# Kernel optimization log

Hardware: AMD Instinct MI355X
Metric: run time of the kernel (lower is better)

The kernel has to match this reference:

```python
import jax, jax.numpy as jnp
import numpy as np

NEG_SLOPE = 0.2  # DenseGATConv default negative_slope


def dense_gat(x, adj, W, att_src, att_dst, bias):
    # x: [B,N,Cin], adj: [B,N,N] (self-loops already added), W: [Cin,H*C]
    B, N, _ = x.shape
    H, C = att_src.shape
    h = (x @ W).reshape(B, N, H, C)
    a_src = jnp.einsum('bnhc,hc->bnh', h, att_src)  # [B,N,H]
    a_dst = jnp.einsum('bnhc,hc->bnh', h, att_dst)
    # alpha[b,i,j,h] = a_src[b,j,h] + a_dst[b,i,h]  (softmax over j, axis=2)
    alpha = a_src[:, None, :, :] + a_dst[:, :, None, :]
    alpha = jnp.where(alpha >= 0, alpha, NEG_SLOPE * alpha)  # leaky_relu
    mask = (adj != 0)[..., None]  # [B,N,N,1]
    alpha = jax.nn.softmax(jnp.where(mask, alpha, -1e30), axis=2)
    out = jnp.einsum('bijh,bjhc->bihc', alpha, h).reshape(B, N, H * C)
    return out + bias


def setup_inputs() -> dict:
    key = jax.random.key(0)
    ks = jax.random.split(key, 8)
    B, N, D = 1, 8192, 128
    x = jax.random.normal(ks[0], (B, N, D), dtype=jnp.float32)
    adj = (jax.random.uniform(ks[1], (B, N, N)) < 0.01).astype(jnp.float32)
    idx = jnp.arange(N)
    adj = adj.at[:, idx, idx].set(1.0)  # DenseGATConv add_loop=True
    s = 1.0 / np.sqrt(D)
    lin = lambda k: jax.random.uniform(k, (D, D), minval=-s, maxval=s, dtype=jnp.float32)
    att = lambda k: jax.random.normal(k, (1, D), dtype=jnp.float32) * 0.1  # heads=1
    return dict(
        x=x, adj=adj,
        W0=lin(ks[2]), att_src0=att(ks[3]), att_dst0=att(ks[4]), b0=jnp.zeros((D,), jnp.float32),
        W1=lin(ks[5]), att_src1=att(ks[6]), att_dst1=att(ks[7]), b1=jnp.zeros((D,), jnp.float32),
    )


def reference(x, adj, W0, att_src0, att_dst0, b0, W1, att_src1, att_dst1, b1):
    out0 = dense_gat(x, adj, W0, att_src0, att_dst0, b0)
    out0 = jax.nn.relu(out0)  # relu_layers_index = [0]
    out1 = dense_gat(out0, adj, W1, att_src1, att_dst1, b1)
    # dropout_rate = 0 -> dropout is identity; squeeze batch dim as in block
    return (out0[0], out1[0])
```

## Files before the change

### kernel.cpp

```cpp
#include <hip/hip_runtime.h>

#define MAXDEG 192
#define NEG_SLOPE 0.2f
#define D 128

__device__ __forceinline__ float bf2f(unsigned short u) {
    return __uint_as_float(((unsigned)u) << 16);
}
__device__ __forceinline__ unsigned short f2bf(float f) {
    unsigned u = __float_as_uint(f);
    return (unsigned short)((u + 0x7fffu + ((u >> 16) & 1u)) >> 16);
}
__device__ __forceinline__ unsigned pack2bf(float x, float y) {
    return (unsigned)f2bf(x) | ((unsigned)f2bf(y) << 16);
}
__device__ __forceinline__ int is_f32(const void* adj) {
    return ((const unsigned*)adj)[0] == 0x3F800000u;
}

__device__ __forceinline__ void ell_group(
        int g, const void* __restrict__ adj, int N, int f32m,
        unsigned short* __restrict__ cols, int* __restrict__ deg,
        int* __restrict__ cnt ) {
    const int w = threadIdx.x >> 6, lane = threadIdx.x & 63;
    const int row = g * 4 + w;
    if (lane == 0) cnt[w] = 0;
    __syncthreads();
    unsigned short* crow = cols + (size_t)row * MAXDEG;
    if (f32m) {
        const float4* arow = (const float4*)((const float*)adj + (size_t)row * N);
        const int nv = N / 4;
        for (int v = lane; v < nv; v += 128) {
            float4 u0 = arow[v];
            float4 u1 = arow[v + 64];
            const unsigned* a0 = (const unsigned*)&u0;
            const unsigned* a1 = (const unsigned*)&u1;
            #pragma unroll
            for (int e = 0; e < 4; e++)
                if (a0[e]) { int p = atomicAdd(&cnt[w], 1); if (p < MAXDEG) crow[p] = (unsigned short)(v * 4 + e); }
            #pragma unroll
            for (int e = 0; e < 4; e++)
                if (a1[e]) { int p = atomicAdd(&cnt[w], 1); if (p < MAXDEG) crow[p] = (unsigned short)((v + 64) * 4 + e); }
        }
    } else {
        const uint4* arow = (const uint4*)((const unsigned short*)adj + (size_t)row * N);
        const int nv = N / 8;
        for (int v = lane; v < nv; v += 128) {
            uint4 u0 = arow[v];
            uint4 u1 = arow[v + 64];
            const unsigned short* s0 = (const unsigned short*)&u0;
            const unsigned short* s1 = (const unsigned short*)&u1;
            #pragma unroll
            for (int e = 0; e < 8; e++)
                if (s0[e]) { int p = atomicAdd(&cnt[w], 1); if (p < MAXDEG) crow[p] = (unsigned short)(v * 8 + e); }
            #pragma unroll
            for (int e = 0; e < 8; e++)
                if (s1[e]) { int p = atomicAdd(&cnt[w], 1); if (p < MAXDEG) crow[p] = (unsigned short)((v + 64) * 8 + e); }
        }
    }
    __syncthreads();
    if (lane == 0) deg[row] = cnt[w] < MAXDEG ? cnt[w] : MAXDEG;
}

__device__ __forceinline__ void gemm_tile32(
        int t, const void* __restrict__ A, const void* __restrict__ W,
        int aF, int f32m, const void* __restrict__ attS, const void* __restrict__ attD,
        unsigned short* __restrict__ Hb, float* __restrict__ asrc, float* __restrict__ adst,
        float* __restrict__ smem) {
    float* xs = smem;
    float* ws = smem + 4096;
    const int tid = threadIdx.x;
    const size_t row0 = (size_t)t * 32;

    if (aF) {
        const float4* av = (const float4*)((const float*)A + row0 * D);
        float4* xl = (float4*)xs;
        #pragma unroll
        for (int k = 0; k < 4; k++) xl[tid + 256 * k] = av[tid + 256 * k];
    } else {
        const uint4* av = (const uint4*)((const unsigned short*)A + row0 * D);
        #pragma unroll
        for (int k = 0; k < 2; k++) {
            uint4 u = av[tid + 256 * k];
            const unsigned short* us = (const unsigned short*)&u;
            #pragma unroll
            for (int e = 0; e < 8; e++) xs[(tid + 256 * k) * 8 + e] = bf2f(us[e]);
        }
    }

    const int tx = tid & 31, ty = tid >> 5;
    const int c0 = tx * 4, r0 = ty * 4;
    float acc[4][4] = {};
    for (int p = 0; p < 4; p++) {
        __syncthreads();
        if (f32m) {
            const float4* wv = (const float4*)((const float*)W + (size_t)p * 32 * D);
            float4* wl = (float4*)ws;
            #pragma unroll
            for (int k = 0; k < 4; k++) wl[tid + 256 * k] = wv[tid + 256 * k];
        } else {
            const uint4* wv = (const uint4*)((const unsigned short*)W + (size_t)p * 32 * D);
            #pragma unroll
            for (int k = 0; k < 2; k++) {
                uint4 u = wv[tid + 256 * k];
                const unsigned short* us = (const unsigned short*)&u;
                #pragma unroll
                for (int e = 0; e < 8; e++) ws[(tid + 256 * k) * 8 + e] = bf2f(us[e]);
            }
        }
        __syncthreads();
        #pragma unroll 8
        for (int k = 0; k < 32; k++) {
            float4 wv = *(const float4*)&ws[k * D + c0];
            #pragma unroll
            for (int i = 0; i < 4; i++) {
                float xv = xs[(r0 + i) * D + p * 32 + k];
                acc[i][0] += xv * wv.x; acc[i][1] += xv * wv.y;
                acc[i][2] += xv * wv.z; acc[i][3] += xv * wv.w;
            }
        }
    }
    #pragma unroll
    for (int i = 0; i < 4; i++) {
        ushort4 hv;
        hv.x = f2bf(acc[i][0]); hv.y = f2bf(acc[i][1]);
        hv.z = f2bf(acc[i][2]); hv.w = f2bf(acc[i][3]);
        *(ushort4*)&Hb[(row0 + r0 + i) * D + c0] = hv;
    }

    float aSv[4], aDv[4];
    #pragma unroll
    for (int j = 0; j < 4; j++) {
        aSv[j] = f32m ? ((const float*)attS)[c0 + j] : bf2f(((const unsigned short*)attS)[c0 + j]);
        aDv[j] = f32m ? ((const float*)attD)[c0 + j] : bf2f(((const unsigned short*)attD)[c0 + j]);
    }
    #pragma unroll
    for (int i = 0; i < 4; i++) {
        float s = acc[i][0] * aSv[0] + acc[i][1] * aSv[1] + acc[i][2] * aSv[2] + acc[i][3] * aSv[3];
        float d = acc[i][0] * aDv[0] + acc[i][1] * aDv[1] + acc[i][2] * aDv[2] + acc[i][3] * aDv[3];
        #pragma unroll
        for (int off = 16; off > 0; off >>= 1) {
            s += __shfl_down(s, off, 32);
            d += __shfl_down(d, off, 32);
        }
        if (tx == 0) {
            asrc[row0 + r0 + i] = s;
            adst[row0 + r0 + i] = d;
        }
    }
}

__device__ __forceinline__ float2 agg_row_bf(
        int row, const unsigned short* __restrict__ Hb,
        const float* __restrict__ asrc, float ai,
        const unsigned short* __restrict__ crow, int d,
        const void* __restrict__ bias, int f32m, int relu,
        float* __restrict__ scn, unsigned short* __restrict__ sjj, int lane) {
    const int s0 = lane, s1 = lane + 64, s2 = lane + 128;
    unsigned short j0 = 0, j1 = 0, j2 = 0;
    float e0 = -3e38f, e1 = -3e38f, e2 = -3e38f;
    if (s0 < d) { j0 = crow[s0]; float e = asrc[j0] + ai; e0 = (e >= 0.f) ? e : NEG_SLOPE * e; }
    if (s1 < d) { j1 = crow[s1]; float e = asrc[j1] + ai; e1 = (e >= 0.f) ? e : NEG_SLOPE * e; }
    if (s2 < d) { j2 = crow[s2]; float e = asrc[j2] + ai; e2 = (e >= 0.f) ? e : NEG_SLOPE * e; }
    float m = fmaxf(e0, fmaxf(e1, e2));
    #pragma unroll
    for (int off = 1; off < 64; off <<= 1) m = fmaxf(m, __shfl_xor(m, off));
    float p0 = (s0 < d) ? __expf(e0 - m) : 0.f;
    float p1 = (s1 < d) ? __expf(e1 - m) : 0.f;
    float p2 = (s2 < d) ? __expf(e2 - m) : 0.f;
    float l = p0 + p1 + p2;
    #pragma unroll
    for (int off = 1; off < 64; off <<= 1) l += __shfl_xor(l, off);
    const float invl = 1.f / l;
    scn[s0] = p0 * invl; sjj[s0] = j0;
    scn[s1] = p1 * invl; sjj[s1] = j1;
    scn[s2] = p2 * invl; sjj[s2] = j2;

    const unsigned* H2 = (const unsigned*)Hb;
    float ax[8], ay[8];
    #pragma unroll
    for (int u = 0; u < 8; u++) { ax[u] = 0.f; ay[u] = 0.f; }
    int k = 0;
    for (; k + 7 < d; k += 8) {
        int jj[8]; float ww[8]; unsigned vv[8];
        #pragma unroll
        for (int u = 0; u < 8; u++) { jj[u] = sjj[k + u]; ww[u] = scn[k + u]; }
        #pragma unroll
        for (int u = 0; u < 8; u++) vv[u] = H2[(size_t)jj[u] * 64 + lane];
        #pragma unroll
        for (int u = 0; u < 8; u++) {
            ax[u] += ww[u] * bf2f((unsigned short)(vv[u] & 0xffff));
            ay[u] += ww[u] * bf2f((unsigned short)(vv[u] >> 16));
        }
    }
    for (; k < d; k++) {
        const int j = sjj[k];
        const float wk = scn[k];
        unsigned v = H2[(size_t)j * 64 + lane];
        ax[0] += wk * bf2f((unsigned short)(v & 0xffff));
        ay[0] += wk * bf2f((unsigned short)(v >> 16));
    }
    #pragma unroll
    for (int u = 1; u < 8; u++) { ax[0] += ax[u]; ay[0] += ay[u]; }

    const int c0 = lane * 2;
    const float bx = f32m ? ((const float*)bias)[c0]     : bf2f(((const unsigned short*)bias)[c0]);
    const float by = f32m ? ((const float*)bias)[c0 + 1] : bf2f(((const unsigned short*)bias)[c0 + 1]);
    float vx = ax[0] + bx, vy = ay[0] + by;
    if (relu) { vx = fmaxf(vx, 0.f); vy = fmaxf(vy, 0.f); }
    return make_float2(vx, vy);
}

__global__ __launch_bounds__(256) void ell_gemm0(
        const void* __restrict__ x, const void* __restrict__ adj,
        const void* __restrict__ W0, const void* __restrict__ aS0,
        const void* __restrict__ aD0, int N,
        unsigned short* __restrict__ cols, int* __restrict__ deg,
        unsigned short* __restrict__ h, float* __restrict__ asrc, float* __restrict__ adst) {
    __shared__ float smem[8192];
    const int bid = blockIdx.x;
    const int f32m = is_f32(adj);
    const int GT = N / 32;
    if (bid < GT)
        gemm_tile32(bid, x, W0, f32m, f32m, aS0, aD0, h, asrc, adst, smem);
    else
        ell_group(bid - GT, adj, N, f32m, cols, deg, (int*)smem);
}

__global__ __launch_bounds__(256) void agg0_gemm1(
        const unsigned short* __restrict__ h,
        const float* __restrict__ asrc0, const float* __restrict__ adst0,
        const unsigned short* __restrict__ cols, const int* __restrict__ deg,
        const void* __restrict__ b0, const void* __restrict__ W1,
        const void* __restrict__ aS1, const void* __restrict__ aD1,
        const void* __restrict__ adjFlag, void* __restrict__ out,
        unsigned short* __restrict__ h2,
        float* __restrict__ asrc1, float* __restrict__ adst1, int N) {
    __shared__ float xs[8 * D];
    __shared__ float wstage[32 * D];
    __shared__ float scnA[4 * MAXDEG];
    __shared__ unsigned short sjjA[4 * MAXDEG];
    const int tid = threadIdx.x;
    const int w = tid >> 6, lane = tid & 63;
    const int f32m = is_f32(adjFlag);

    #pragma unroll
    for (int pass = 0; pass < 2; pass++) {
        const int rl = pass * 4 + w;
        const int row = blockIdx.x * 8 + rl;
        float2 v = agg_row_bf(row, h, asrc0, adst0[row],
                              cols + (size_t)row * MAXDEG, deg[row],
                              b0, f32m, 1,
                              scnA + w * MAXDEG, sjjA + w * MAXDEG, lane);
        xs[rl * D + 2 * lane]     = v.x;
        xs[rl * D + 2 * lane + 1] = v.y;
        if (f32m) ((float2*)out)[(size_t)row * 64 + lane] = v;
        else      ((unsigned*)out)[(size_t)row * 64 + lane] = pack2bf(v.x, v.y);
    }

    const int tx = tid & 31, ty = tid >> 5;
    const int c0 = tx * 4;
    float acc[4] = {};
    for (int p = 0; p < 4; p++) {
        __syncthreads();
        if (f32m) {
            const float4* wv = (const float4*)((const float*)W1 + (size_t)p * 32 * D);
            float4* wl = (float4*)wstage;
            #pragma unroll
            for (int k = 0; k < 4; k++) wl[tid + 256 * k] = wv[tid + 256 * k];
        } else {
            const uint4* wv = (const uint4*)((const unsigned short*)W1 + (size_t)p * 32 * D);
            #pragma unroll
            for (int k = 0; k < 2; k++) {
                uint4 u = wv[tid + 256 * k];
                const unsigned short* us = (const unsigned short*)&u;
                #pragma unroll
                for (int e = 0; e < 8; e++) wstage[(tid + 256 * k) * 8 + e] = bf2f(us[e]);
            }
        }
        __syncthreads();
        #pragma unroll 8
        for (int k = 0; k < 32; k++) {
            float4 wv = *(const float4*)&wstage[k * D + c0];
            float xv = xs[ty * D + p * 32 + k];
            acc[0] += xv * wv.x; acc[1] += xv * wv.y;
            acc[2] += xv * wv.z; acc[3] += xv * wv.w;
        }
    }
    const size_t row1 = (size_t)blockIdx.x * 8 + ty;
    ushort4 hv;
    hv.x = f2bf(acc[0]); hv.y = f2bf(acc[1]); hv.z = f2bf(acc[2]); hv.w = f2bf(acc[3]);
    *(ushort4*)&h2[row1 * D + c0] = hv;

    float aSv[4], aDv[4];
    #pragma unroll
    for (int j = 0; j < 4; j++) {
        aSv[j] = f32m ? ((const float*)aS1)[c0 + j] : bf2f(((const unsigned short*)aS1)[c0 + j]);
        aDv[j] = f32m ? ((const float*)aD1)[c0 + j] : bf2f(((const unsigned short*)aD1)[c0 + j]);
    }
    float s = acc[0] * aSv[0] + acc[1] * aSv[1] + acc[2] * aSv[2] + acc[3] * aSv[3];
    float d = acc[0] * aDv[0] + acc[1] * aDv[1] + acc[2] * aDv[2] + acc[3] * aDv[3];
    #pragma unroll
    for (int off = 16; off > 0; off >>= 1) {
        s += __shfl_down(s, off, 32);
        d += __shfl_down(d, off, 32);
    }
    if (tx == 0) {
        asrc1[row1] = s;
        adst1[row1] = d;
    }
}

__global__ __launch_bounds__(256) void aggregate1(
        const unsigned short* __restrict__ h2,
        const float* __restrict__ asrc1, const float* __restrict__ adst1,
        const unsigned short* __restrict__ cols, const int* __restrict__ deg,
        const void* __restrict__ b1, const void* __restrict__ adjFlag,
        void* __restrict__ out, int N) {
    __shared__ float scnA[4 * MAXDEG];
    __shared__ unsigned short sjjA[4 * MAXDEG];
    const int w = threadIdx.x >> 6, lane = threadIdx.x & 63;
    const int row = blockIdx.x * 4 + w;
    const int f32m = is_f32(adjFlag);
    float2 v = agg_row_bf(row, h2, asrc1, adst1[row],
                          cols + (size_t)row * MAXDEG, deg[row],
                          b1, f32m, 0,
                          scnA + w * MAXDEG, sjjA + w * MAXDEG, lane);
    const size_t off2 = (size_t)N * 64;
    if (f32m) ((float2*)out)[off2 + (size_t)row * 64 + lane] = v;
    else      ((unsigned*)out)[off2 + (size_t)row * 64 + lane] = pack2bf(v.x, v.y);
}

extern "C" void kernel_launch(void* const* d_in, const int* in_sizes, int n_in,
                              void* d_out, int out_size, void* d_ws, size_t ws_size,
                              hipStream_t stream) {
    const int N = in_sizes[0] / D;

    char* w = (char*)d_ws;
    int* deg             = (int*)w;            w += (size_t)N * sizeof(int);
    unsigned short* cols = (unsigned short*)w; w += (size_t)N * MAXDEG * sizeof(unsigned short);
    unsigned short* h    = (unsigned short*)w; w += (size_t)N * D * sizeof(unsigned short);
    unsigned short* h2   = (unsigned short*)w; w += (size_t)N * D * sizeof(unsigned short);
    float* asrc0         = (float*)w;          w += (size_t)N * sizeof(float);
    float* adst0         = (float*)w;          w += (size_t)N * sizeof(float);
    float* asrc1         = (float*)w;          w += (size_t)N * sizeof(float);
    float* adst1         = (float*)w;

    const void* adj = d_in[1];

    ell_gemm0<<<N / 32 + N / 4, 256, 0, stream>>>(
        d_in[0], adj, d_in[2], d_in[3], d_in[4], N, cols, deg, h, asrc0, adst0);

    agg0_gemm1<<<N / 8, 256, 0, stream>>>(
        h, asrc0, adst0, cols, deg, d_in[5], d_in[6], d_in[7], d_in[8],
        adj, d_out, h2, asrc1, adst1, N);

    aggregate1<<<N / 4, 256, 0, stream>>>(
        h2, asrc1, adst1, cols, deg, d_in[9], adj, d_out, N);
}
```

Before: 419.8 us.

## Use ballot-based ELL compaction and half-wave 8-byte gathers in aggregation

Neighbor-list construction replaces per-element LDS atomics and block barriers with wave ballot plus popcount prefix, which gives deterministic, ordered column slots. The aggregation loop now splits each wave into two halves. Each half handles alternate neighbors with 8-byte loads covering four channels, and the halves are combined with a cross-half shuffle. This aims to cut atomic contention and sync overhead in the dense adjacency scan and to widen gather loads. The cost is a final reduction and half the lanes sitting idle during output writes.

```diff
diff --git a/kernel.cpp b/kernel.cpp
--- a/kernel.cpp
+++ b/kernel.cpp
@@ -20,46 +20,68 @@
 
 __device__ __forceinline__ void ell_group(
         int g, const void* __restrict__ adj, int N, int f32m,
-        unsigned short* __restrict__ cols, int* __restrict__ deg,
-        int* __restrict__ cnt ) {
+        unsigned short* __restrict__ cols, int* __restrict__ deg) {
     const int w = threadIdx.x >> 6, lane = threadIdx.x & 63;
     const int row = g * 4 + w;
-    if (lane == 0) cnt[w] = 0;
-    __syncthreads();
     unsigned short* crow = cols + (size_t)row * MAXDEG;
+    const unsigned long long lt = (1ull << lane) - 1ull;
+    int cnt = 0;
     if (f32m) {
         const float4* arow = (const float4*)((const float*)adj + (size_t)row * N);
         const int nv = N / 4;
-        for (int v = lane; v < nv; v += 128) {
-            float4 u0 = arow[v];
-            float4 u1 = arow[v + 64];
+        for (int c = lane; c < nv; c += 128) {
+            float4 u0 = arow[c];
+            float4 u1 = arow[c + 64];
             const unsigned* a0 = (const unsigned*)&u0;
             const unsigned* a1 = (const unsigned*)&u1;
             #pragma unroll
-            for (int e = 0; e < 4; e++)
-                if (a0[e]) { int p = atomicAdd(&cnt[w], 1); if (p < MAXDEG) crow[p] = (unsigned short)(v * 4 + e); }
-            #pragma unroll
-            for (int e = 0; e < 4; e++)
-                if (a1[e]) { int p = atomicAdd(&cnt[w], 1); if (p < MAXDEG) crow[p] = (unsigned short)((v + 64) * 4 + e); }
+            for (int e = 0; e < 4; e++) {
+                unsigned long long m = __ballot(a0[e] != 0u);
+                if (a0[e]) {
+                    int p = cnt + __popcll(m & lt);
+                    if (p < MAXDEG) crow[p] = (unsigned short)(c * 4 + e);
+                }
+                cnt += __popcll(m);
+            }
+            #pragma unroll
+            for (int e = 0; e < 4; e++) {
+                unsigned long long m = __ballot(a1[e] != 0u);
+                if (a1[e]) {
+                    int p = cnt + __popcll(m & lt);
+                    if (p < MAXDEG) crow[p] = (unsigned short)((c + 64) * 4 + e);
+                }
+                cnt += __popcll(m);
+            }
         }
     } else {
         const uint4* arow = (const uint4*)((const unsigned short*)adj + (size_t)row * N);
         const int nv = N / 8;
-        for (int v = lane; v < nv; v += 128) {
-            uint4 u0 = arow[v];
-            uint4 u1 = arow[v + 64];
+        for (int c = lane; c < nv; c += 128) {
+            uint4 u0 = arow[c];
+            uint4 u1 = arow[c + 64];
             const unsigned short* s0 = (const unsigned short*)&u0;
             const unsigned short* s1 = (const unsigned short*)&u1;
             #pragma unroll
-            for (int e = 0; e < 8; e++)
-                if (s0[e]) { int p = atomicAdd(&cnt[w], 1); if (p < MAXDEG) crow[p] = (unsigned short)(v * 8 + e); }
-            #pragma unroll
-            for (int e = 0; e < 8; e++)
-                if (s1[e]) { int p = atomicAdd(&cnt[w], 1); if (p < MAXDEG) crow[p] = (unsigned short)((v + 64) * 8 + e); }
-        }
-    }
-    __syncthreads();
-    if (lane == 0) deg[row] = cnt[w] < MAXDEG ? cnt[w] : MAXDEG;
+            for (int e = 0; e < 8; e++) {
+                unsigned long long m = __ballot(s0[e] != 0);
+                if (s0[e]) {
+                    int p = cnt + __popcll(m & lt);
+                    if (p < MAXDEG) crow[p] = (unsigned short)(c * 8 + e);
+                }
+                cnt += __popcll(m);
+            }
+            #pragma unroll
+            for (int e = 0; e < 8; e++) {
+                unsigned long long m = __ballot(s1[e] != 0);
+                if (s1[e]) {
+                    int p = cnt + __popcll(m & lt);
+                    if (p < MAXDEG) crow[p] = (unsigned short)((c + 64) * 8 + e);
+                }
+                cnt += __popcll(m);
+            }
+        }
+    }
+    if (lane == 0) deg[row] = cnt < MAXDEG ? cnt : MAXDEG;
 }
 
 __device__ __forceinline__ void gemm_tile32(
@@ -150,8 +172,8 @@
     }
 }
 
-__device__ __forceinline__ float2 agg_row_bf(
-        int row, const unsigned short* __restrict__ Hb,
+__device__ __forceinline__ float4 agg_row_bf(
+        const unsigned short* __restrict__ Hb,
         const float* __restrict__ asrc, float ai,
         const unsigned short* __restrict__ crow, int d,
         const void* __restrict__ bias, int f32m, int relu,
@@ -176,39 +198,57 @@
     scn[s1] = p1 * invl; sjj[s1] = j1;
     scn[s2] = p2 * invl; sjj[s2] = j2;
 
-    const unsigned* H2 = (const unsigned*)Hb;
-    float ax[8], ay[8];
-    #pragma unroll
-    for (int u = 0; u < 8; u++) { ax[u] = 0.f; ay[u] = 0.f; }
+    const int half = lane >> 5, hl = lane & 31;
+    const uint2* H4 = (const uint2*)Hb;
+    float a0 = 0.f, a1 = 0.f, a2 = 0.f, a3 = 0.f;
     int k = 0;
-    for (; k + 7 < d; k += 8) {
-        int jj[8]; float ww[8]; unsigned vv[8];
-        #pragma unroll
-        for (int u = 0; u < 8; u++) { jj[u] = sjj[k + u]; ww[u] = scn[k + u]; }
-        #pragma unroll
-        for (int u = 0; u < 8; u++) vv[u] = H2[(size_t)jj[u] * 64 + lane];
+    for (; k + 15 < d; k += 16) {
+        unsigned jj[8]; float ww[8]; uint2 vv[8];
         #pragma unroll
         for (int u = 0; u < 8; u++) {
-            ax[u] += ww[u] * bf2f((unsigned short)(vv[u] & 0xffff));
-            ay[u] += ww[u] * bf2f((unsigned short)(vv[u] >> 16));
-        }
-    }
-    for (; k < d; k++) {
-        const int j = sjj[k];
-        const float wk = scn[k];
-        unsigned v = H2[(size_t)j * 64 + lane];
-        ax[0] += wk * bf2f((unsigned short)(v & 0xffff));
-        ay[0] += wk * bf2f((unsigned short)(v >> 16));
-    }
-    #pragma unroll
-    for (int u = 1; u < 8; u++) { ax[0] += ax[u]; ay[0] += ay[u]; }
-
-    const int c0 = lane * 2;
-    const float bx = f32m ? ((const float*)bias)[c0]     : bf2f(((const unsigned short*)bias)[c0]);
-    const float by = f32m ? ((const float*)bias)[c0 + 1] : bf2f(((const unsigned short*)bias)[c0 + 1]);
-    float vx = ax[0] + bx, vy = ay[0] + by;
-    if (relu) { vx = fmaxf(vx, 0.f); vy = fmaxf(vy, 0.f); }
-    return make_float2(vx, vy);
+            const int slot = k + 2 * u + half;
+            jj[u] = sjj[slot]; ww[u] = scn[slot];
+        }
+        #pragma unroll
+        for (int u = 0; u < 8; u++) vv[u] = H4[jj[u] * 32u + (unsigned)hl];
+        #pragma unroll
+        for (int u = 0; u < 8; u++) {
+            a0 += ww[u] * bf2f((unsigned short)(vv[u].x & 0xffffu));
+            a1 += ww[u] * bf2f((unsigned short)(vv[u].x >> 16));
+            a2 += ww[u] * bf2f((unsigned short)(vv[u].y & 0xffffu));
+            a3 += ww[u] * bf2f((unsigned short)(vv[u].y >> 16));
+        }
+    }
+    for (int s = k + half; s < d; s += 2) {
+        const unsigned j = sjj[s];
+        const float wk = scn[s];
+        uint2 v = H4[j * 32u + (unsigned)hl];
+        a0 += wk * bf2f((unsigned short)(v.x & 0xffffu));
+        a1 += wk * bf2f((unsigned short)(v.x >> 16));
+        a2 += wk * bf2f((unsigned short)(v.y & 0xffffu));
+        a3 += wk * bf2f((unsigned short)(v.y >> 16));
+    }
+    a0 += __shfl_xor(a0, 32);
+    a1 += __shfl_xor(a1, 32);
+    a2 += __shfl_xor(a2, 32);
+    a3 += __shfl_xor(a3, 32);
+
+    float4 r;
+    if (f32m) {
+        float4 b = ((const float4*)bias)[hl];
+        r = make_float4(a0 + b.x, a1 + b.y, a2 + b.z, a3 + b.w);
+    } else {
+        uint2 b = ((const uint2*)bias)[hl];
+        r = make_float4(a0 + bf2f((unsigned short)(b.x & 0xffffu)),
+                        a1 + bf2f((unsigned short)(b.x >> 16)),
+                        a2 + bf2f((unsigned short)(b.y & 0xffffu)),
+                        a3 + bf2f((unsigned short)(b.y >> 16)));
+    }
+    if (relu) {
+        r.x = fmaxf(r.x, 0.f); r.y = fmaxf(r.y, 0.f);
+        r.z = fmaxf(r.z, 0.f); r.w = fmaxf(r.w, 0.f);
+    }
+    return r;
 }
 
 __global__ __launch_bounds__(256) void ell_gemm0(
@@ -224,7 +264,7 @@
     if (bid < GT)
         gemm_tile32(bid, x, W0, f32m, f32m, aS0, aD0, h, asrc, adst, smem);
     else
-        ell_group(bid - GT, adj, N, f32m, cols, deg, (int*)smem);
+        ell_group(bid - GT, adj, N, f32m, cols, deg);
 }
 
 __global__ __launch_bounds__(256) void agg0_gemm1(
@@ -248,14 +288,16 @@
     for (int pass = 0; pass < 2; pass++) {
         const int rl = pass * 4 + w;
         const int row = blockIdx.x * 8 + rl;
-        float2 v = agg_row_bf(row, h, asrc0, adst0[row],
+        float4 v = agg_row_bf(h, asrc0, adst0[row],
                               cols + (size_t)row * MAXDEG, deg[row],
                               b0, f32m, 1,
                               scnA + w * MAXDEG, sjjA + w * MAXDEG, lane);
-        xs[rl * D + 2 * lane]     = v.x;
-        xs[rl * D + 2 * lane + 1] = v.y;
-        if (f32m) ((float2*)out)[(size_t)row * 64 + lane] = v;
-        else      ((unsigned*)out)[(size_t)row * 64 + lane] = pack2bf(v.x, v.y);
+        if (lane < 32) {
+            *(float4*)&xs[rl * D + 4 * lane] = v;
+            if (f32m) ((float4*)out)[(size_t)row * 32 + lane] = v;
+            else      ((uint2*)out)[(size_t)row * 32 + lane] =
+                          make_uint2(pack2bf(v.x, v.y), pack2bf(v.z, v.w));
+        }
     }
 
     const int tx = tid & 31, ty = tid >> 5;
@@ -322,13 +364,16 @@
     const int w = threadIdx.x >> 6, lane = threadIdx.x & 63;
     const int row = blockIdx.x * 4 + w;
     const int f32m = is_f32(adjFlag);
-    float2 v = agg_row_bf(row, h2, asrc1, adst1[row],
+    float4 v = agg_row_bf(h2, asrc1, adst1[row],
                           cols + (size_t)row * MAXDEG, deg[row],
                           b1, f32m, 0,
                           scnA + w * MAXDEG, sjjA + w * MAXDEG, lane);
-    const size_t off2 = (size_t)N * 64;
-    if (f32m) ((float2*)out)[off2 + (size_t)row * 64 + lane] = v;
-    else      ((unsigned*)out)[off2 + (size_t)row * 64 + lane] = pack2bf(v.x, v.y);
+    const size_t off4 = (size_t)N * 32;
+    if (lane < 32) {
+        if (f32m) ((float4*)out)[off4 + (size_t)row * 32 + lane] = v;
+        else      ((uint2*)out)[off4 + (size_t)row * 32 + lane] =
+                      make_uint2(pack2bf(v.x, v.y), pack2bf(v.z, v.w));
+    }
 }
 
 extern "C" void kernel_launch(void* const* d_in, const int* in_sizes, int n_in,
```

Result: no change. 419.8 us (-0.0%).
